# Kernel optimization log

Hardware: AMD Instinct MI355X
Metric: run time of the kernel (lower is better)

## Reference

```python
import jax, jax.numpy as jnp
import numpy as np

B, N, E, T = 32768, 6, 6, 2  # batch graphs, nodes, edges (ring), edge types
H, DIN = 128, 3


def _ring_rel():
    # off_diag[i, (i+1)%N] = 1 -> edge e: sender i, receiver (i+1)%N
    send = np.arange(N)
    recv = (np.arange(N) + 1) % N
    eye = np.eye(N, dtype=np.float32)
    return jnp.asarray(eye[recv]), jnp.asarray(eye[send])  # rel_rec, rel_send [E,N]


def setup_inputs() -> dict:
    key = jax.random.key(0)
    ks = iter(jax.random.split(key, 40))
    rn = lambda shape, s=0.1: jax.random.normal(next(ks), shape, jnp.float32) * s
    rel_rec, rel_send = _ring_rel()
    inp = {
        'x': rn((B, N, DIN), 1.0),
        'rel_rec': rel_rec, 'rel_send': rel_send,
        'e1w1': rn((DIN, H)), 'e1b1': jnp.full((H,), 0.1), 'e1w2': rn((H, H)), 'e1b2': jnp.full((H,), 0.1),
        'e2w1': rn((2 * H, H)), 'e2b1': jnp.full((H,), 0.1), 'e2w2': rn((H, H)), 'e2b2': jnp.full((H,), 0.1),
        'e3w1': rn((H, H)), 'e3b1': jnp.full((H,), 0.1), 'e3w2': rn((H, H)), 'e3b2': jnp.full((H,), 0.1),
        'e4w1': rn((2 * H, H)), 'e4b1': jnp.full((H,), 0.1), 'e4w2': rn((H, H)), 'e4b2': jnp.full((H,), 0.1),
        'ew_out': rn((H, T)), 'eb_out': jnp.full((T,), 0.1),
        'd_msg_w1': rn((T, 2 * DIN, H)), 'd_msg_b1': rn((T, H), 0.01),
        'd_msg_w2': rn((T, H, H)), 'd_msg_b2': rn((T, H), 0.01),
        'd_out_w1': rn((DIN + H, H)), 'd_out_b1': rn((H,), 0.01),
        'd_out_w2': rn((H, H)), 'd_out_b2': rn((H,), 0.01),
        'd_out_w3': rn((H, DIN)), 'd_out_b3': rn((DIN,), 0.01),
    }
    return inp


def _mlp(h, w1, b1, w2, b2):
    # two-layer ELU MLP (dropout inactive at eval)
    return jax.nn.elu(jax.nn.elu(h @ w1 + b1) @ w2 + b2)


def reference(x, rel_rec, rel_send,
              e1w1, e1b1, e1w2, e1b2, e2w1, e2b1, e2w2, e2b2,
              e3w1, e3b1, e3w2, e3b2, e4w1, e4b1, e4w2, e4b2,
              ew_out, eb_out,
              d_msg_w1, d_msg_b1, d_msg_w2, d_msg_b2,
              d_out_w1, d_out_b1, d_out_w2, d_out_b2, d_out_w3, d_out_b3):
    node2edge = lambda h: jnp.concatenate(
        [jnp.einsum('en,bnh->beh', rel_rec, h), jnp.einsum('en,bnh->beh', rel_send, h)], axis=-1)

    # ---- GraphEncoder (factor=False) ----
    h = _mlp(x, e1w1, e1b1, e1w2, e1b2)                      # [B,N,H]
    he = _mlp(node2edge(h), e2w1, e2b1, e2w2, e2b2)          # [B,E,H]
    h2 = _mlp(he, e3w1, e3b1, e3w2, e3b2)                    # [B,E,H]
    h3 = _mlp(jnp.concatenate([h2, he], -1), e4w1, e4b1, e4w2, e4b2)
    logits = h3 @ ew_out + eb_out                            # [B,E,T]
    rel_type = jax.nn.softmax(logits, axis=-1)               # edge-type weights

    # ---- GraphDecoder single step (skip_first=False) ----
    recv = jnp.einsum('en,bnd->bed', rel_rec, x)             # [B,E,DIN]
    send = jnp.einsum('en,bnd->bed', rel_send, x)
    pre_msg = jnp.concatenate([recv, send], axis=-1)         # [B,E,2*DIN]
    # batched per-edge-type MLP: one grouped GEMM instead of a python loop of layers
    m = jax.nn.relu(jnp.einsum('bei,tih->bteh', pre_msg, d_msg_w1) + d_msg_b1[None, :, None, :])
    m = jax.nn.relu(jnp.einsum('bteh,tho->bteo', m, d_msg_w2) + d_msg_b2[None, :, None, :])
    all_msgs = jnp.einsum('bteh,bet->beh', m, rel_type)      # weight + accumulate over types
    agg_msgs = jnp.einsum('beh,en->bnh', all_msgs, rel_rec)  # edge -> node aggregation

    aug = jnp.concatenate([x, agg_msgs], axis=-1)            # [B,N,DIN+H]
    p = jax.nn.relu(aug @ d_out_w1 + d_out_b1)
    p = jax.nn.relu(p @ d_out_w2 + d_out_b2)
    p = p @ d_out_w3 + d_out_b3
    return x + p                                             # [B,N,DIN]
```

## Files before the change

### kernel.cpp

```cpp
#include <hip/hip_runtime.h>
#include <hip/hip_bf16.h>

typedef __bf16 bf16x8 __attribute__((ext_vector_type(8)));
typedef __bf16 bf16x4 __attribute__((ext_vector_type(4)));
typedef float floatx4 __attribute__((ext_vector_type(4)));

#define LDW 128
#define PXW 8

#define SWZ(row, col) ((row) * LDW + ((col) ^ (((row) & 7) << 3)))

#define O_E1W2  0
#define O_E2W1  16384
#define O_E2W2  49152
#define O_E3W1  65536
#define O_E3W2  81920
#define O_E4W1  98304
#define O_E4W2  131072
#define O_DM2T0 147456
#define O_DM2T1 163840
#define O_DO1   180224
#define O_DO2   196608
#define O_EWOUT 212992
#define O_DW3   215040
#define O_E1W1P 217088
#define O_M1T0P 221184
#define O_M1T1P 225280
#define O_DO1XP 229376
#define WS_ELEMS 233472

__global__ void prep_kernel(const float* e1w2, const float* e2w1, const float* e2w2,
    const float* e3w1, const float* e3w2, const float* e4w1, const float* e4w2,
    const float* dmsg2, const float* dout1, const float* dout2,
    const float* ew_out, const float* dout_w3, const float* e1w1,
    const float* dmsg_w1, __hip_bfloat16* ws) {
  int idx = blockIdx.x * 256 + threadIdx.x;
  if (idx >= WS_ELEMS) return;
  float v;
  if (idx < O_E2W1)      { int l = idx;           v = e1w2[(l & 127) * 128 + (l >> 7)]; }
  else if (idx < O_E2W2) { int l = idx - O_E2W1;  v = e2w1[(l & 255) * 128 + (l >> 8)]; }
  else if (idx < O_E3W1) { int l = idx - O_E2W2;  v = e2w2[(l & 127) * 128 + (l >> 7)]; }
  else if (idx < O_E3W2) { int l = idx - O_E3W1;  v = e3w1[(l & 127) * 128 + (l >> 7)]; }
  else if (idx < O_E4W1) { int l = idx - O_E3W2;  v = e3w2[(l & 127) * 128 + (l >> 7)]; }
  else if (idx < O_E4W2) { int l = idx - O_E4W1;  v = e4w1[(l & 255) * 128 + (l >> 8)]; }
  else if (idx < O_DM2T0){ int l = idx - O_E4W2;  v = e4w2[(l & 127) * 128 + (l >> 7)]; }
  else if (idx < O_DM2T1){ int l = idx - O_DM2T0; v = dmsg2[(l & 127) * 128 + (l >> 7)]; }
  else if (idx < O_DO1)  { int l = idx - O_DM2T1; v = dmsg2[16384 + (l & 127) * 128 + (l >> 7)]; }
  else if (idx < O_DO2)  { int l = idx - O_DO1;   v = dout1[384 + (l & 127) * 128 + (l >> 7)]; }
  else if (idx < O_EWOUT){ int l = idx - O_DO2;   v = dout2[(l & 127) * 128 + (l >> 7)]; }
  else if (idx < O_DW3)  { int l = idx - O_EWOUT; int n = l >> 7;
                           v = (n < 2) ? ew_out[(l & 127) * 2 + n] : 0.f; }
  else if (idx < O_E1W1P){ int l = idx - O_DW3;   int n = l >> 7;
                           v = (n < 3) ? dout_w3[(l & 127) * 3 + n] : 0.f; }
  else if (idx < O_M1T0P){ int l = idx - O_E1W1P; int n = l >> 5, c = l & 31;
                           v = (c >= 3 && c < 6) ? e1w1[(c - 3) * 128 + n] : 0.f; }
  else if (idx < O_M1T1P){ int l = idx - O_M1T0P; int n = l >> 5, c = l & 31;
                           v = (c < 6) ? dmsg_w1[c * 128 + n] : 0.f; }
  else if (idx < O_DO1XP){ int l = idx - O_M1T1P; int n = l >> 5, c = l & 31;
                           v = (c < 6) ? dmsg_w1[768 + c * 128 + n] : 0.f; }
  else                   { int l = idx - O_DO1XP; int n = l >> 5, c = l & 31;
                           v = (c >= 3 && c < 6) ? dout1[(c - 3) * 128 + n] : 0.f; }
  ws[idx] = __float2bfloat16(v);
}

struct W4 { bf16x8 b[4]; };
struct W8 { bf16x8 b[8]; };
union PK { bf16x4 v; __hip_bfloat16 h[4]; };

__global__ __launch_bounds__(512, 4) void nri_fused(
    const float* __restrict__ x,
    const float* __restrict__ e1b1, const float* __restrict__ e1b2,
    const float* __restrict__ e2b1, const float* __restrict__ e2b2,
    const float* __restrict__ e3b1, const float* __restrict__ e3b2,
    const float* __restrict__ e4b1, const float* __restrict__ e4b2,
    const float* __restrict__ eb_out,
    const float* __restrict__ dmsg_b1, const float* __restrict__ dmsg_b2,
    const float* __restrict__ dout_b1, const float* __restrict__ dout_b2,
    const float* __restrict__ dout_b3,
    const __bf16* __restrict__ wt, float* __restrict__ out)
{
  const int tid  = threadIdx.x;
  const int wave = tid >> 6;
  const int lane = tid & 63;
  const int nl   = lane & 15;
  const int quad = lane >> 4;
  const int colb = wave * 16 + nl;
  const int cq   = wave * 16 + quad * 4;
  const int gx   = blockIdx.x * 288;

  __shared__ __align__(16) __hip_bfloat16 bufA[96 * LDW];
  __shared__ __align__(16) __hip_bfloat16 bufB[96 * LDW];
  __shared__ __align__(16) __hip_bfloat16 pxb[96 * PXW];
  __shared__ __hip_bfloat16 rtw[192];

  floatx4 b_s1 = *(const floatx4*)(e1b1 + cq);
  bf16x8 wk_s1 = *(const bf16x8*)(wt + O_E1W1P + colb * 32 + quad * 8);

  for (int i = tid; i < 96 * PXW; i += 512) {
    int row = i >> 3, c = i & 7;
    int e = row % 6;
    float v = 0.f;
    if (c < 3)      { int rr = row + ((e == 5) ? -5 : 1); v = x[gx + rr * 3 + c]; }
    else if (c < 6) v = x[gx + row * 3 + (c - 3)];
    pxb[i] = __float2bfloat16(v);
  }
  __syncthreads();

  auto initv = [&](floatx4 (&a)[6], floatx4 bv) {
#pragma unroll
    for (int mt = 0; mt < 6; ++mt) a[mt] = bv;
  };

  auto loadW128 = [&](int wofs) {
    W4 w;
    const __bf16* p = wt + wofs + colb * 128 + quad * 8;
#pragma unroll
    for (int ks = 0; ks < 4; ++ks) w.b[ks] = *(const bf16x8*)(p + ks * 32);
    return w;
  };
  auto loadW256 = [&](int wofs) {
    W8 w;
    const __bf16* p = wt + wofs + colb * 256 + quad * 8;
#pragma unroll
    for (int ks = 0; ks < 8; ++ks) w.b[ks] = *(const bf16x8*)(p + ks * 32);
    return w;
  };
  auto loadW256half = [&](int wofs, int kh) {
    W4 w;
    const __bf16* p = wt + wofs + colb * 256 + kh * 128 + quad * 8;
#pragma unroll
    for (int ks = 0; ks < 4; ++ks) w.b[ks] = *(const bf16x8*)(p + ks * 32);
    return w;
  };

  auto gemmP = [&](floatx4 (&acc)[6], const W4& w, const __hip_bfloat16* in) {
    const __bf16* ab = (const __bf16*)(const void*)in;
#pragma unroll
    for (int ks = 0; ks < 4; ++ks) {
      int kk = ks * 32 + quad * 8;
#pragma unroll
      for (int mt = 0; mt < 6; ++mt) {
        bf16x8 b = *(const bf16x8*)(ab + SWZ(mt * 16 + nl, kk));
        acc[mt] = __builtin_amdgcn_mfma_f32_16x16x32_bf16(w.b[ks], b, acc[mt], 0, 0, 0);
      }
    }
  };
  auto gemmP2 = [&](floatx4 (&accA)[6], const W4& wA, floatx4 (&accB)[6],
                    const W4& wB, const __hip_bfloat16* in) {
    const __bf16* ab = (const __bf16*)(const void*)in;
#pragma unroll
    for (int ks = 0; ks < 4; ++ks) {
      int kk = ks * 32 + quad * 8;
#pragma unroll
      for (int mt = 0; mt < 6; ++mt) {
        bf16x8 b = *(const bf16x8*)(ab + SWZ(mt * 16 + nl, kk));
        accA[mt] = __builtin_amdgcn_mfma_f32_16x16x32_bf16(wA.b[ks], b, accA[mt], 0, 0, 0);
        accB[mt] = __builtin_amdgcn_mfma_f32_16x16x32_bf16(wB.b[ks], b, accB[mt], 0, 0, 0);
      }
    }
  };
  auto gemm256P = [&](floatx4 (&acc)[6], const W8& w, const __hip_bfloat16* in) {
    int row0[6], row1[6];
#pragma unroll
    for (int mt = 0; mt < 6; ++mt) {
      int r = mt * 16 + nl;
      row1[mt] = r;
      int e = r % 6;
      row0[mt] = r + ((e == 5) ? -5 : 1);
    }
    const __bf16* ab = (const __bf16*)(const void*)in;
#pragma unroll
    for (int ks = 0; ks < 8; ++ks) {
      int kk = (ks & 3) * 32 + quad * 8;
      const int* rows = (ks < 4) ? row0 : row1;
#pragma unroll
      for (int mt = 0; mt < 6; ++mt) {
        bf16x8 b = *(const bf16x8*)(ab + SWZ(rows[mt], kk));
        acc[mt] = __builtin_amdgcn_mfma_f32_16x16x32_bf16(w.b[ks], b, acc[mt], 0, 0, 0);
      }
    }
  };
  auto gemm32 = [&](floatx4 (&acc)[6], bf16x8 wfrag) {
    const __bf16* pb = (const __bf16*)(const void*)pxb;
#pragma unroll
    for (int mt = 0; mt < 6; ++mt) {
      bf16x8 b = {0, 0, 0, 0, 0, 0, 0, 0};
      if (quad == 0) b = *(const bf16x8*)(pb + (mt * 16 + nl) * PXW);
      acc[mt] = __builtin_amdgcn_mfma_f32_16x16x32_bf16(wfrag, b, acc[mt], 0, 0, 0);
    }
  };
  auto store_act = [&](floatx4 (&acc)[6], int act, __hip_bfloat16* ob) {
#pragma unroll
    for (int mt = 0; mt < 6; ++mt) {
      PK p;
#pragma unroll
      for (int r = 0; r < 4; ++r) {
        float z = acc[mt][r];
        if (act == 1) z = (z > 0.f) ? z : (__expf(z) - 1.f);
        else z = fmaxf(z, 0.f);
        p.h[r] = __float2bfloat16(z);
      }
      *(bf16x4*)((__bf16*)(void*)ob + SWZ(mt * 16 + nl, cq)) = p.v;
    }
  };

  floatx4 acc[6], acc2[6];

  initv(acc, b_s1); gemm32(acc, wk_s1);
  W4 w2 = loadW128(O_E1W2);
  floatx4 b_s2 = *(const floatx4*)(e1b2 + cq);
  store_act(acc, 1, bufA);
  __syncthreads();
  initv(acc, b_s2); gemmP(acc, w2, bufA);
  W8 w3 = loadW256(O_E2W1);
  floatx4 b_s3 = *(const floatx4*)(e2b1 + cq);
  store_act(acc, 1, bufB);
  __syncthreads();
  initv(acc, b_s3); gemm256P(acc, w3, bufB);
  W4 w4 = loadW128(O_E2W2);
  floatx4 b_s4 = *(const floatx4*)(e2b2 + cq);
  store_act(acc, 1, bufA);
  __syncthreads();
  initv(acc, b_s4); gemmP(acc, w4, bufA);
  W4 w5 = loadW128(O_E3W1);
  W4 w5b = loadW256half(O_E4W1, 1);
  floatx4 b_s5 = *(const floatx4*)(e3b1 + cq);
  floatx4 b2_s5 = *(const floatx4*)(e4b1 + cq);
  store_act(acc, 1, bufB);
  __syncthreads();
  initv(acc, b_s5); initv(acc2, b2_s5);
  gemmP2(acc, w5, acc2, w5b, bufB);
  W4 w6 = loadW128(O_E3W2);
  floatx4 b_s6 = *(const floatx4*)(e3b2 + cq);
  store_act(acc, 1, bufA);
  __syncthreads();
  initv(acc, b_s6); gemmP(acc, w6, bufA);
  W4 w7 = loadW256half(O_E4W1, 0);
  store_act(acc, 1, bufB);
  __syncthreads();
  gemmP(acc2, w7, bufB);
  W4 w8 = loadW128(O_E4W2);
  floatx4 b_s8 = *(const floatx4*)(e4b2 + cq);
  store_act(acc2, 1, bufA);
  __syncthreads();
  initv(acc, b_s8); gemmP(acc, w8, bufA);
  float ebv = (nl < 2) ? eb_out[nl] : 0.f;
  bf16x8 wk10a = *(const bf16x8*)(wt + O_M1T0P + colb * 32 + quad * 8);
  bf16x8 wk10b = *(const bf16x8*)(wt + O_M1T1P + colb * 32 + quad * 8);
  floatx4 b_m0 = *(const floatx4*)(dmsg_b1 + cq);
  floatx4 b_m1 = *(const floatx4*)(dmsg_b1 + 128 + cq);
  store_act(acc, 1, bufB);
  __syncthreads();

  if (wave < 6) {
    int tile = wave;
    floatx4 lg = {ebv, ebv, ebv, ebv};
    const __bf16* ab = (const __bf16*)(const void*)bufB;
    const __bf16* wp = wt + O_EWOUT + nl * 128 + quad * 8;
#pragma unroll
    for (int ks = 0; ks < 4; ++ks) {
      bf16x8 a = *(const bf16x8*)(ab + SWZ(tile * 16 + nl, ks * 32 + quad * 8));
      bf16x8 b = *(const bf16x8*)(wp + ks * 32);
      lg = __builtin_amdgcn_mfma_f32_16x16x32_bf16(a, b, lg, 0, 0, 0);
    }
    if (nl < 2) {
#pragma unroll
      for (int r = 0; r < 4; ++r)
        rtw[(tile * 16 + quad * 4 + r) * 2 + nl] = __float2bfloat16(lg[r]);
    }
  }
  __syncthreads();

  if (tid < 96) {
    float l0 = __bfloat162float(rtw[tid * 2]);
    float l1 = __bfloat162float(rtw[tid * 2 + 1]);
    float mx = fmaxf(l0, l1);
    float ea = __expf(l0 - mx), eb = __expf(l1 - mx);
    float inv = 1.f / (ea + eb);
    rtw[tid * 2] = __float2bfloat16(ea * inv);
    rtw[tid * 2 + 1] = __float2bfloat16(eb * inv);
  }
  initv(acc, b_m0);  gemm32(acc, wk10a);  store_act(acc, 2, bufA);
  initv(acc2, b_m1); gemm32(acc2, wk10b); store_act(acc2, 2, bufB);
  W4 wm0 = loadW128(O_DM2T0);
  W4 wm1 = loadW128(O_DM2T1);
  floatx4 b_d0 = *(const floatx4*)(dmsg_b2 + cq);
  floatx4 b_d1 = *(const floatx4*)(dmsg_b2 + 128 + cq);
  __syncthreads();

  initv(acc, b_d0);  gemmP(acc, wm0, bufA);
  initv(acc2, b_d1); gemmP(acc2, wm1, bufB);
#pragma unroll
  for (int mt = 0; mt < 6; ++mt) {
    int row = mt * 16 + nl;
    float r0 = __bfloat162float(rtw[row * 2]);
    float r1 = __bfloat162float(rtw[row * 2 + 1]);
#pragma unroll
    for (int r = 0; r < 4; ++r)
      acc[mt][r] = r0 * fmaxf(acc[mt][r], 0.f) + r1 * fmaxf(acc2[mt][r], 0.f);
  }
  W4 wd1 = loadW128(O_DO1);
  bf16x8 wk13 = *(const bf16x8*)(wt + O_DO1XP + colb * 32 + quad * 8);
  floatx4 b_p1 = *(const floatx4*)(dout_b1 + cq);
  __syncthreads();

#pragma unroll
  for (int mt = 0; mt < 6; ++mt) {
    int row = mt * 16 + nl;
    int e = row % 6;
    int orow = row + ((e == 5) ? -5 : 1);
    PK p;
#pragma unroll
    for (int r = 0; r < 4; ++r) p.h[r] = __float2bfloat16(acc[mt][r]);
    *(bf16x4*)((__bf16*)(void*)bufA + SWZ(orow, cq)) = p.v;
  }
  __syncthreads();

  initv(acc, b_p1); gemmP(acc, wd1, bufA); gemm32(acc, wk13);
  W4 wd2 = loadW128(O_DO2);
  floatx4 b_p2 = *(const floatx4*)(dout_b2 + cq);
  store_act(acc, 2, bufB);
  __syncthreads();
  initv(acc, b_p2); gemmP(acc, wd2, bufB);
  float b3v = (nl < 3) ? dout_b3[nl] : 0.f;
  store_act(acc, 2, bufA);
  __syncthreads();

  if (wave < 6) {
    int tile = wave;
    floatx4 d = {b3v, b3v, b3v, b3v};
    const __bf16* ab = (const __bf16*)(const void*)bufA;
    const __bf16* wp = wt + O_DW3 + nl * 128 + quad * 8;
#pragma unroll
    for (int ks = 0; ks < 4; ++ks) {
      bf16x8 a = *(const bf16x8*)(ab + SWZ(tile * 16 + nl, ks * 32 + quad * 8));
      bf16x8 b = *(const bf16x8*)(wp + ks * 32);
      d = __builtin_amdgcn_mfma_f32_16x16x32_bf16(a, b, d, 0, 0, 0);
    }
    if (nl < 3) {
#pragma unroll
      for (int r = 0; r < 4; ++r) {
        int row = tile * 16 + quad * 4 + r;
        out[gx + row * 3 + nl] = x[gx + row * 3 + nl] + d[r];
      }
    }
  }
}

extern "C" void kernel_launch(void* const* d_in, const int* in_sizes, int n_in,
                              void* d_out, int out_size, void* d_ws, size_t ws_size,
                              hipStream_t stream) {
  const float* x       = (const float*)d_in[0];
  const float* e1w1    = (const float*)d_in[3];
  const float* e1b1    = (const float*)d_in[4];
  const float* e1w2    = (const float*)d_in[5];
  const float* e1b2    = (const float*)d_in[6];
  const float* e2w1    = (const float*)d_in[7];
  const float* e2b1    = (const float*)d_in[8];
  const float* e2w2    = (const float*)d_in[9];
  const float* e2b2    = (const float*)d_in[10];
  const float* e3w1    = (const float*)d_in[11];
  const float* e3b1    = (const float*)d_in[12];
  const float* e3w2    = (const float*)d_in[13];
  const float* e3b2    = (const float*)d_in[14];
  const float* e4w1    = (const float*)d_in[15];
  const float* e4b1    = (const float*)d_in[16];
  const float* e4w2    = (const float*)d_in[17];
  const float* e4b2    = (const float*)d_in[18];
  const float* ew_out  = (const float*)d_in[19];
  const float* eb_out  = (const float*)d_in[20];
  const float* dmsg_w1 = (const float*)d_in[21];
  const float* dmsg_b1 = (const float*)d_in[22];
  const float* dmsg_w2 = (const float*)d_in[23];
  const float* dmsg_b2 = (const float*)d_in[24];
  const float* dout_w1 = (const float*)d_in[25];
  const float* dout_b1 = (const float*)d_in[26];
  const float* dout_w2 = (const float*)d_in[27];
  const float* dout_b2 = (const float*)d_in[28];
  const float* dout_w3 = (const float*)d_in[29];
  const float* dout_b3 = (const float*)d_in[30];

  prep_kernel<<<(WS_ELEMS + 255) / 256, 256, 0, stream>>>(
      e1w2, e2w1, e2w2, e3w1, e3w2, e4w1, e4w2, dmsg_w2, dout_w1, dout_w2,
      ew_out, dout_w3, e1w1, dmsg_w1, (__hip_bfloat16*)d_ws);

  nri_fused<<<32768 / 16, 512, 0, stream>>>(
      x, e1b1, e1b2, e2b1, e2b2, e3b1, e3b2, e4b1, e4b2, eb_out,
      dmsg_b1, dmsg_b2, dout_b1, dout_b2, dout_b3,
      (const __bf16*)d_ws, (float*)d_out);
}
```

Before: 261.3 us.

## Retile wave work into 2x4 grid of 48-row by 32-column tiles

Changes each wave's output tile from all 96 rows by 16 columns to 48 rows by 32 columns, using a 2x4 wave grid. Each LDS activation fragment now feeds two MFMAs, which halves LDS reads per MFMA, while each wave holds weight fragments for two column tiles. The 256-wide input GEMM is split into two half-K GEMMs with a row-shift flag. This costs more weight registers per wave and doubles global weight-fragment loads per row-half, which may pressure occupancy under the 512x4 launch bounds.

Result: slower. 414.4 us (+58.6%).

```diff
diff --git a/kernel.cpp b/kernel.cpp
--- a/kernel.cpp
+++ b/kernel.cpp
@@ -63,8 +63,9 @@
   ws[idx] = __float2bfloat16(v);
 }
 
-struct W4 { bf16x8 b[4]; };
-struct W8 { bf16x8 b[8]; };
+struct W2 { bf16x8 b[2][4]; };
+struct WK { bf16x8 k[2]; };
+struct B2 { floatx4 v[2]; };
 union PK { bf16x4 v; __hip_bfloat16 h[4]; };
 
 __global__ __launch_bounds__(512, 4) void nri_fused(
@@ -84,8 +85,10 @@
   const int lane = tid & 63;
   const int nl   = lane & 15;
   const int quad = lane >> 4;
-  const int colb = wave * 16 + nl;
-  const int cq   = wave * 16 + quad * 4;
+  const int rw   = wave >> 2;
+  const int cw   = wave & 3;
+  const int rb   = rw * 48;
+  const int cb   = cw * 32;
   const int gx   = blockIdx.x * 288;
 
   __shared__ __align__(16) __hip_bfloat16 bufA[96 * LDW];
@@ -93,8 +96,12 @@
   __shared__ __align__(16) __hip_bfloat16 pxb[96 * PXW];
   __shared__ __hip_bfloat16 rtw[192];
 
-  floatx4 b_s1 = *(const floatx4*)(e1b1 + cq);
-  bf16x8 wk_s1 = *(const bf16x8*)(wt + O_E1W1P + colb * 32 + quad * 8);
+  B2 b_s1 = { *(const floatx4*)(e1b1 + cb + quad * 4),
+              *(const floatx4*)(e1b1 + cb + 16 + quad * 4) };
+  WK wk_s1;
+#pragma unroll
+  for (int ct = 0; ct < 2; ++ct)
+    wk_s1.k[ct] = *(const bf16x8*)(wt + O_E1W1P + (cb + ct * 16 + nl) * 32 + quad * 8);
 
   for (int i = tid; i < 96 * PXW; i += 512) {
     int row = i >> 3, c = i & 7;
@@ -106,150 +113,166 @@
   }
   __syncthreads();
 
-  auto initv = [&](floatx4 (&a)[6], floatx4 bv) {
-#pragma unroll
-    for (int mt = 0; mt < 6; ++mt) a[mt] = bv;
-  };
-
+  auto ldb = [&](const float* p, int ofs) {
+    B2 r;
+    r.v[0] = *(const floatx4*)(p + ofs + cb + quad * 4);
+    r.v[1] = *(const floatx4*)(p + ofs + cb + 16 + quad * 4);
+    return r;
+  };
+  auto initv = [&](floatx4 (&a)[3][2], const B2& b) {
+#pragma unroll
+    for (int mt = 0; mt < 3; ++mt)
+#pragma unroll
+      for (int ct = 0; ct < 2; ++ct) a[mt][ct] = b.v[ct];
+  };
   auto loadW128 = [&](int wofs) {
-    W4 w;
-    const __bf16* p = wt + wofs + colb * 128 + quad * 8;
-#pragma unroll
-    for (int ks = 0; ks < 4; ++ks) w.b[ks] = *(const bf16x8*)(p + ks * 32);
+    W2 w;
+#pragma unroll
+    for (int ct = 0; ct < 2; ++ct) {
+      const __bf16* p = wt + wofs + (cb + ct * 16 + nl) * 128 + quad * 8;
+#pragma unroll
+      for (int ks = 0; ks < 4; ++ks) w.b[ct][ks] = *(const bf16x8*)(p + ks * 32);
+    }
     return w;
   };
-  auto loadW256 = [&](int wofs) {
-    W8 w;
-    const __bf16* p = wt + wofs + colb * 256 + quad * 8;
-#pragma unroll
-    for (int ks = 0; ks < 8; ++ks) w.b[ks] = *(const bf16x8*)(p + ks * 32);
+  auto loadW256h = [&](int wofs, int kh) {
+    W2 w;
+#pragma unroll
+    for (int ct = 0; ct < 2; ++ct) {
+      const __bf16* p = wt + wofs + (cb + ct * 16 + nl) * 256 + kh * 128 + quad * 8;
+#pragma unroll
+      for (int ks = 0; ks < 4; ++ks) w.b[ct][ks] = *(const bf16x8*)(p + ks * 32);
+    }
     return w;
   };
-  auto loadW256half = [&](int wofs, int kh) {
-    W4 w;
-    const __bf16* p = wt + wofs + colb * 256 + kh * 128 + quad * 8;
-#pragma unroll
-    for (int ks = 0; ks < 4; ++ks) w.b[ks] = *(const bf16x8*)(p + ks * 32);
+  auto loadWK = [&](int wofs) {
+    WK w;
+#pragma unroll
+    for (int ct = 0; ct < 2; ++ct)
+      w.k[ct] = *(const bf16x8*)(wt + wofs + (cb + ct * 16 + nl) * 32 + quad * 8);
     return w;
   };
 
-  auto gemmP = [&](floatx4 (&acc)[6], const W4& w, const __hip_bfloat16* in) {
+  auto gemmP = [&](floatx4 (&acc)[3][2], const W2& w, const __hip_bfloat16* in,
+                   bool shift) {
     const __bf16* ab = (const __bf16*)(const void*)in;
+    int rows[3];
+#pragma unroll
+    for (int mt = 0; mt < 3; ++mt) {
+      int r = rb + mt * 16 + nl;
+      rows[mt] = shift ? (r + ((r % 6 == 5) ? -5 : 1)) : r;
+    }
 #pragma unroll
     for (int ks = 0; ks < 4; ++ks) {
       int kk = ks * 32 + quad * 8;
 #pragma unroll
-      for (int mt = 0; mt < 6; ++mt) {
-        bf16x8 b = *(const bf16x8*)(ab + SWZ(mt * 16 + nl, kk));
-        acc[mt] = __builtin_amdgcn_mfma_f32_16x16x32_bf16(w.b[ks], b, acc[mt], 0, 0, 0);
+      for (int mt = 0; mt < 3; ++mt) {
+        bf16x8 b = *(const bf16x8*)(ab + SWZ(rows[mt], kk));
+#pragma unroll
+        for (int ct = 0; ct < 2; ++ct)
+          acc[mt][ct] = __builtin_amdgcn_mfma_f32_16x16x32_bf16(w.b[ct][ks], b, acc[mt][ct], 0, 0, 0);
       }
     }
   };
-  auto gemmP2 = [&](floatx4 (&accA)[6], const W4& wA, floatx4 (&accB)[6],
-                    const W4& wB, const __hip_bfloat16* in) {
+  auto gemmP2 = [&](floatx4 (&a1)[3][2], const W2& w1, floatx4 (&a2)[3][2],
+                    const W2& w2v, const __hip_bfloat16* in) {
     const __bf16* ab = (const __bf16*)(const void*)in;
 #pragma unroll
     for (int ks = 0; ks < 4; ++ks) {
       int kk = ks * 32 + quad * 8;
 #pragma unroll
-      for (int mt = 0; mt < 6; ++mt) {
-        bf16x8 b = *(const bf16x8*)(ab + SWZ(mt * 16 + nl, kk));
-        accA[mt] = __builtin_amdgcn_mfma_f32_16x16x32_bf16(wA.b[ks], b, accA[mt], 0, 0, 0);
-        accB[mt] = __builtin_amdgcn_mfma_f32_16x16x32_bf16(wB.b[ks], b, accB[mt], 0, 0, 0);
+      for (int mt = 0; mt < 3; ++mt) {
+        bf16x8 b = *(const bf16x8*)(ab + SWZ(rb + mt * 16 + nl, kk));
+#pragma unroll
+        for (int ct = 0; ct < 2; ++ct) {
+          a1[mt][ct] = __builtin_amdgcn_mfma_f32_16x16x32_bf16(w1.b[ct][ks], b, a1[mt][ct], 0, 0, 0);
+          a2[mt][ct] = __builtin_amdgcn_mfma_f32_16x16x32_bf16(w2v.b[ct][ks], b, a2[mt][ct], 0, 0, 0);
+        }
       }
     }
   };
-  auto gemm256P = [&](floatx4 (&acc)[6], const W8& w, const __hip_bfloat16* in) {
-    int row0[6], row1[6];
-#pragma unroll
-    for (int mt = 0; mt < 6; ++mt) {
-      int r = mt * 16 + nl;
-      row1[mt] = r;
-      int e = r % 6;
-      row0[mt] = r + ((e == 5) ? -5 : 1);
-    }
-    const __bf16* ab = (const __bf16*)(const void*)in;
-#pragma unroll
-    for (int ks = 0; ks < 8; ++ks) {
-      int kk = (ks & 3) * 32 + quad * 8;
-      const int* rows = (ks < 4) ? row0 : row1;
-#pragma unroll
-      for (int mt = 0; mt < 6; ++mt) {
-        bf16x8 b = *(const bf16x8*)(ab + SWZ(rows[mt], kk));
-        acc[mt] = __builtin_amdgcn_mfma_f32_16x16x32_bf16(w.b[ks], b, acc[mt], 0, 0, 0);
+  auto gemm32 = [&](floatx4 (&acc)[3][2], const WK& w) {
+    const __bf16* pb = (const __bf16*)(const void*)pxb;
+#pragma unroll
+    for (int mt = 0; mt < 3; ++mt) {
+      bf16x8 b = {0, 0, 0, 0, 0, 0, 0, 0};
+      if (quad == 0) b = *(const bf16x8*)(pb + (rb + mt * 16 + nl) * PXW);
+#pragma unroll
+      for (int ct = 0; ct < 2; ++ct)
+        acc[mt][ct] = __builtin_amdgcn_mfma_f32_16x16x32_bf16(w.k[ct], b, acc[mt][ct], 0, 0, 0);
+    }
+  };
+  auto store_act = [&](floatx4 (&acc)[3][2], int act, __hip_bfloat16* ob,
+                       bool shift) {
+#pragma unroll
+    for (int mt = 0; mt < 3; ++mt) {
+      int r = rb + mt * 16 + nl;
+      int row = shift ? (r + ((r % 6 == 5) ? -5 : 1)) : r;
+      int s = (row & 7) << 3;
+#pragma unroll
+      for (int ct = 0; ct < 2; ++ct) {
+        PK p;
+#pragma unroll
+        for (int j = 0; j < 4; ++j) {
+          float z = acc[mt][ct][j];
+          if (act == 1) z = (z > 0.f) ? z : (__expf(z) - 1.f);
+          else if (act == 2) z = fmaxf(z, 0.f);
+          p.h[j] = __float2bfloat16(z);
+        }
+        *(bf16x4*)((__bf16*)(void*)ob + row * LDW + ((cb + ct * 16 + quad * 4) ^ s)) = p.v;
       }
     }
   };
-  auto gemm32 = [&](floatx4 (&acc)[6], bf16x8 wfrag) {
-    const __bf16* pb = (const __bf16*)(const void*)pxb;
-#pragma unroll
-    for (int mt = 0; mt < 6; ++mt) {
-      bf16x8 b = {0, 0, 0, 0, 0, 0, 0, 0};
-      if (quad == 0) b = *(const bf16x8*)(pb + (mt * 16 + nl) * PXW);
-      acc[mt] = __builtin_amdgcn_mfma_f32_16x16x32_bf16(wfrag, b, acc[mt], 0, 0, 0);
-    }
-  };
-  auto store_act = [&](floatx4 (&acc)[6], int act, __hip_bfloat16* ob) {
-#pragma unroll
-    for (int mt = 0; mt < 6; ++mt) {
-      PK p;
-#pragma unroll
-      for (int r = 0; r < 4; ++r) {
-        float z = acc[mt][r];
-        if (act == 1) z = (z > 0.f) ? z : (__expf(z) - 1.f);
-        else z = fmaxf(z, 0.f);
-        p.h[r] = __float2bfloat16(z);
-      }
-      *(bf16x4*)((__bf16*)(void*)ob + SWZ(mt * 16 + nl, cq)) = p.v;
-    }
-  };
-
-  floatx4 acc[6], acc2[6];
+
+  floatx4 acc[3][2], acc2[3][2];
 
   initv(acc, b_s1); gemm32(acc, wk_s1);
-  W4 w2 = loadW128(O_E1W2);
-  floatx4 b_s2 = *(const floatx4*)(e1b2 + cq);
-  store_act(acc, 1, bufA);
-  __syncthreads();
-  initv(acc, b_s2); gemmP(acc, w2, bufA);
-  W8 w3 = loadW256(O_E2W1);
-  floatx4 b_s3 = *(const floatx4*)(e2b1 + cq);
-  store_act(acc, 1, bufB);
-  __syncthreads();
-  initv(acc, b_s3); gemm256P(acc, w3, bufB);
-  W4 w4 = loadW128(O_E2W2);
-  floatx4 b_s4 = *(const floatx4*)(e2b2 + cq);
-  store_act(acc, 1, bufA);
-  __syncthreads();
-  initv(acc, b_s4); gemmP(acc, w4, bufA);
-  W4 w5 = loadW128(O_E3W1);
-  W4 w5b = loadW256half(O_E4W1, 1);
-  floatx4 b_s5 = *(const floatx4*)(e3b1 + cq);
-  floatx4 b2_s5 = *(const floatx4*)(e4b1 + cq);
-  store_act(acc, 1, bufB);
+  W2 w2 = loadW128(O_E1W2);
+  B2 b_s2 = ldb(e1b2, 0);
+  store_act(acc, 1, bufA, false);
+  __syncthreads();
+  initv(acc, b_s2); gemmP(acc, w2, bufA, false);
+  W2 w3a = loadW256h(O_E2W1, 0);
+  B2 b_s3 = ldb(e2b1, 0);
+  store_act(acc, 1, bufB, false);
+  __syncthreads();
+  initv(acc, b_s3);
+  W2 w3b = loadW256h(O_E2W1, 1);
+  gemmP(acc, w3a, bufB, true);
+  gemmP(acc, w3b, bufB, false);
+  W2 w4 = loadW128(O_E2W2);
+  B2 b_s4 = ldb(e2b2, 0);
+  store_act(acc, 1, bufA, false);
+  __syncthreads();
+  initv(acc, b_s4); gemmP(acc, w4, bufA, false);
+  W2 w5 = loadW128(O_E3W1);
+  W2 w5b = loadW256h(O_E4W1, 1);
+  B2 b_s5 = ldb(e3b1, 0);
+  B2 b2_s5 = ldb(e4b1, 0);
+  store_act(acc, 1, bufB, false);
   __syncthreads();
   initv(acc, b_s5); initv(acc2, b2_s5);
   gemmP2(acc, w5, acc2, w5b, bufB);
-  W4 w6 = loadW128(O_E3W2);
-  floatx4 b_s6 = *(const floatx4*)(e3b2 + cq);
-  store_act(acc, 1, bufA);
-  __syncthreads();
-  initv(acc, b_s6); gemmP(acc, w6, bufA);
-  W4 w7 = loadW256half(O_E4W1, 0);
-  store_act(acc, 1, bufB);
-  __syncthreads();
-  gemmP(acc2, w7, bufB);
-  W4 w8 = loadW128(O_E4W2);
-  floatx4 b_s8 = *(const floatx4*)(e4b2 + cq);
-  store_act(acc2, 1, bufA);
-  __syncthreads();
-  initv(acc, b_s8); gemmP(acc, w8, bufA);
+  W2 w6 = loadW128(O_E3W2);
+  B2 b_s6 = ldb(e3b2, 0);
+  store_act(acc, 1, bufA, false);
+  __syncthreads();
+  initv(acc, b_s6); gemmP(acc, w6, bufA, false);
+  W2 w7 = loadW256h(O_E4W1, 0);
+  store_act(acc, 1, bufB, false);
+  __syncthreads();
+  gemmP(acc2, w7, bufB, false);
+  W2 w8 = loadW128(O_E4W2);
+  B2 b_s8 = ldb(e4b2, 0);
+  store_act(acc2, 1, bufA, false);
+  __syncthreads();
+  initv(acc, b_s8); gemmP(acc, w8, bufA, false);
   float ebv = (nl < 2) ? eb_out[nl] : 0.f;
-  bf16x8 wk10a = *(const bf16x8*)(wt + O_M1T0P + colb * 32 + quad * 8);
-  bf16x8 wk10b = *(const bf16x8*)(wt + O_M1T1P + colb * 32 + quad * 8);
-  floatx4 b_m0 = *(const floatx4*)(dmsg_b1 + cq);
-  floatx4 b_m1 = *(const floatx4*)(dmsg_b1 + 128 + cq);
-  store_act(acc, 1, bufB);
+  WK wk10a = loadWK(O_M1T0P);
+  WK wk10b = loadWK(O_M1T1P);
+  B2 b_m0 = ldb(dmsg_b1, 0);
+  B2 b_m1 = ldb(dmsg_b1, 128);
+  store_act(acc, 1, bufB, false);
   __syncthreads();
 
   if (wave < 6) {
@@ -280,50 +303,43 @@
     rtw[tid * 2] = __float2bfloat16(ea * inv);
     rtw[tid * 2 + 1] = __float2bfloat16(eb * inv);
   }
-  initv(acc, b_m0);  gemm32(acc, wk10a);  store_act(acc, 2, bufA);
-  initv(acc2, b_m1); gemm32(acc2, wk10b); store_act(acc2, 2, bufB);
-  W4 wm0 = loadW128(O_DM2T0);
-  W4 wm1 = loadW128(O_DM2T1);
-  floatx4 b_d0 = *(const floatx4*)(dmsg_b2 + cq);
-  floatx4 b_d1 = *(const floatx4*)(dmsg_b2 + 128 + cq);
-  __syncthreads();
-
-  initv(acc, b_d0);  gemmP(acc, wm0, bufA);
-  initv(acc2, b_d1); gemmP(acc2, wm1, bufB);
-#pragma unroll
-  for (int mt = 0; mt < 6; ++mt) {
-    int row = mt * 16 + nl;
+  initv(acc, b_m0);  gemm32(acc, wk10a);  store_act(acc, 2, bufA, false);
+  initv(acc2, b_m1); gemm32(acc2, wk10b); store_act(acc2, 2, bufB, false);
+  W2 wm0 = loadW128(O_DM2T0);
+  W2 wm1 = loadW128(O_DM2T1);
+  B2 b_d0 = ldb(dmsg_b2, 0);
+  B2 b_d1 = ldb(dmsg_b2, 128);
+  __syncthreads();
+
+  initv(acc, b_d0);  gemmP(acc, wm0, bufA, false);
+  initv(acc2, b_d1); gemmP(acc2, wm1, bufB, false);
+#pragma unroll
+  for (int mt = 0; mt < 3; ++mt) {
+    int row = rb + mt * 16 + nl;
     float r0 = __bfloat162float(rtw[row * 2]);
     float r1 = __bfloat162float(rtw[row * 2 + 1]);
 #pragma unroll
-    for (int r = 0; r < 4; ++r)
-      acc[mt][r] = r0 * fmaxf(acc[mt][r], 0.f) + r1 * fmaxf(acc2[mt][r], 0.f);
+    for (int ct = 0; ct < 2; ++ct)
+#pragma unroll
+      for (int j = 0; j < 4; ++j)
+        acc[mt][ct][j] = r0 * fmaxf(acc[mt][ct][j], 0.f) + r1 * fmaxf(acc2[mt][ct][j], 0.f);
   }
-  W4 wd1 = loadW128(O_DO1);
-  bf16x8 wk13 = *(const bf16x8*)(wt + O_DO1XP + colb * 32 + quad * 8);
-  floatx4 b_p1 = *(const floatx4*)(dout_b1 + cq);
-  __syncthreads();
-
-#pragma unroll
-  for (int mt = 0; mt < 6; ++mt) {
-    int row = mt * 16 + nl;
-    int e = row % 6;
-    int orow = row + ((e == 5) ? -5 : 1);
-    PK p;
-#pragma unroll
-    for (int r = 0; r < 4; ++r) p.h[r] = __float2bfloat16(acc[mt][r]);
-    *(bf16x4*)((__bf16*)(void*)bufA + SWZ(orow, cq)) = p.v;
-  }
-  __syncthreads();
-
-  initv(acc, b_p1); gemmP(acc, wd1, bufA); gemm32(acc, wk13);
-  W4 wd2 = loadW128(O_DO2);
-  floatx4 b_p2 = *(const floatx4*)(dout_b2 + cq);
-  store_act(acc, 2, bufB);
-  __syncthreads();
-  initv(acc, b_p2); gemmP(acc, wd2, bufB);
+  W2 wd1 = loadW128(O_DO1);
+  WK wk13 = loadWK(O_DO1XP);
+  B2 b_p1 = ldb(dout_b1, 0);
+  __syncthreads();
+
+  store_act(acc, 0, bufA, true);
+  __syncthreads();
+
+  initv(acc, b_p1); gemmP(acc, wd1, bufA, false); gemm32(acc, wk13);
+  W2 wd2 = loadW128(O_DO2);
+  B2 b_p2 = ldb(dout_b2, 0);
+  store_act(acc, 2, bufB, false);
+  __syncthreads();
+  initv(acc, b_p2); gemmP(acc, wd2, bufB, false);
   float b3v = (nl < 3) ? dout_b3[nl] : 0.f;
-  store_act(acc, 2, bufA);
+  store_act(acc, 2, bufA, false);
   __syncthreads();
 
   if (wave < 6) {
```
